# Performance work log

Hardware: AMD Instinct MI355X
Metric: run time of the kernel (lower is better)

Reference implementation:

```python
import jax, jax.numpy as jnp
import numpy as np

N_EMBD = 768
N_HEAD = 12
HEAD_DIM = N_EMBD // N_HEAD  # 64


def setup_inputs() -> dict:
    key = jax.random.key(0)
    k1, k2, k3 = jax.random.split(key, 3)
    B, S = 4, 2048
    x = jax.random.normal(k1, (B, S, N_EMBD), dtype=jnp.float32)
    W_attn = jax.random.normal(k2, (N_EMBD, 3 * N_EMBD), dtype=jnp.float32) * 0.02
    b_attn = jax.random.normal(k3, (3 * N_EMBD,), dtype=jnp.float32) * 0.02
    return {"x": x, "W_attn": W_attn, "b_attn": b_attn}


def reference(x, W_attn, b_attn):
    B, S, E = x.shape
    H, D = N_HEAD, HEAD_DIM
    # fused QKV projection (torch Linear: x @ W^T + b; here W_attn stored as [E, 3E])
    qkv = x @ W_attn + b_attn  # [B, S, 3E]
    q, k, v = jnp.split(qkv, 3, axis=-1)
    q = q.reshape(B, S, H, D)
    k = k.reshape(B, S, H, D)
    v = v.reshape(B, S, H, D)
    scale = 1.0 / np.sqrt(D).astype(np.float32)
    scores = jnp.einsum('bqhd,bkhd->bhqk', q, k) * scale  # [B, H, S, S]
    causal = jnp.tril(jnp.ones((S, S), dtype=bool))
    # ReLU attention nonlinearity (no softmax); masked entries -> 0
    att = jnp.where(causal, jnp.maximum(scores, 0.0), 0.0)
    y = jnp.einsum('bhqk,bkhd->bqhd', att, v)  # [B, S, H, D]
    return y.reshape(B, S, E)
```

## Files before the change

kernel.cpp:

```cpp
#include <hip/hip_runtime.h>

typedef __attribute__((ext_vector_type(8))) short short8;
typedef __attribute__((ext_vector_type(4))) short short4v;
typedef __attribute__((ext_vector_type(4))) float floatx4;
typedef __attribute__((ext_vector_type(2))) unsigned int uint2v;

#define S_LEN 2048
#define NH 12
#define HD 64
#define EMB 768
#define E3 2304

__device__ __forceinline__ unsigned short f2bf(float f) {
    unsigned int u = __builtin_bit_cast(unsigned int, f);
    u += 0x7FFFu + ((u >> 16) & 1u);
    return (unsigned short)(u >> 16);
}

__device__ __forceinline__ unsigned int pack2bf(float a, float b) {
#if __has_builtin(__builtin_amdgcn_cvt_pk_bf16_f32)
    typedef __attribute__((ext_vector_type(2))) short short2v;
    short2v r = __builtin_amdgcn_cvt_pk_bf16_f32(a, b);
    return __builtin_bit_cast(unsigned int, r);
#else
    return (unsigned int)f2bf(a) | ((unsigned int)f2bf(b) << 16);
#endif
}

__device__ __forceinline__ void gl_lds16(const void* g, void* l) {
    __builtin_amdgcn_global_load_lds(
        (const __attribute__((address_space(1))) unsigned int*)g,
        (__attribute__((address_space(3))) unsigned int*)l, 16, 0, 0);
}

__global__ __launch_bounds__(256) void conv_fused(const float* __restrict__ x,
                                                  ushort* __restrict__ xb,
                                                  const float* __restrict__ W,
                                                  ushort* __restrict__ Wt) {
    int tid = threadIdx.x;
    if (blockIdx.x < 6144) {
        int i = (blockIdx.x * 256 + tid) * 4;
        float4 f = *(const float4*)(x + i);
        ushort4 o;
        o.x = f2bf(f.x); o.y = f2bf(f.y); o.z = f2bf(f.z); o.w = f2bf(f.w);
        *(ushort4*)(xb + i) = o;
    } else {
        __shared__ float tile[32][33];
        int b2 = blockIdx.x - 6144;
        int n0 = (b2 % 72) * 32, k0 = (b2 / 72) * 32;
        int tx = tid & 31, ty = tid >> 5;
        for (int i = 0; i < 4; i++)
            tile[ty + i * 8][tx] = W[(size_t)(k0 + ty + i * 8) * E3 + n0 + tx];
        __syncthreads();
        for (int i = 0; i < 4; i++)
            Wt[(size_t)(n0 + ty + i * 8) * EMB + k0 + tx] = f2bf(tile[tx][ty + i * 8]);
    }
}

__global__ __launch_bounds__(256) void qkv_gemm(const ushort* __restrict__ Xb,
                                                const ushort* __restrict__ Wt,
                                                const float* __restrict__ bias,
                                                ushort* __restrict__ QKb,
                                                ushort* __restrict__ Vt) {
    __shared__ ushort lds[16896];
    char* ldsb = (char*)lds;
    int tid  = threadIdx.x;
    int wv = tid >> 6, lane = tid & 63;
    int l15 = lane & 15, quad = lane >> 4;
    int r8 = lane >> 3, cc = lane & 7;
    int wm = wv >> 1, wn = wv & 1;
    int m0 = blockIdx.x * 128, n0 = blockIdx.y * 128;

    floatx4 acc[4][4] = {};

    const char* ag = (const char*)(Xb + (size_t)m0 * EMB)
                   + (wv * 32 + r8) * 1536 + (cc ^ r8) * 16;
    const char* bgp = (const char*)(Wt + (size_t)n0 * EMB)
                   + (wv * 32 + r8) * 1536 + (cc ^ r8) * 16;
    int ast = (wv * 32) * 128;
    int bst = 16384 + (wv * 32) * 128;
    int afo[2], bfo[2];
    for (int ch = 0; ch < 2; ch++) {
        int sw = ((ch * 4 + quad) ^ (l15 & 7)) * 16;
        afo[ch] = wm * 8192 + l15 * 128 + sw;
        bfo[ch] = 16384 + wn * 8192 + l15 * 128 + sw;
    }

    for (int k0 = 0; k0 < 12; k0++) {
        __syncthreads();
        for (int i = 0; i < 4; i++) {
            gl_lds16(ag + i * 12288, ldsb + ast + i * 1024);
            gl_lds16(bgp + i * 12288, ldsb + bst + i * 1024);
        }
        ag += 128;  bgp += 128;
        __syncthreads();
        for (int ch = 0; ch < 2; ch++) {
            short8 af[4], bf[4];
            for (int mi = 0; mi < 4; mi++)
                af[mi] = *(const short8*)(ldsb + afo[ch] + mi * 2048);
            for (int ni = 0; ni < 4; ni++)
                bf[ni] = *(const short8*)(ldsb + bfo[ch] + ni * 2048);
            for (int mi = 0; mi < 4; mi++)
                for (int ni = 0; ni < 4; ni++)
                    acc[mi][ni] = __builtin_amdgcn_mfma_f32_16x16x32_bf16(
                        af[mi], bf[ni], acc[mi][ni], 0, 0, 0);
        }
    }

    __syncthreads();
    int seg = n0 / EMB;
    if (seg < 2) {
        float scale = (seg == 0) ? 0.125f : 1.0f;
        for (int ni = 0; ni < 4; ni++) {
            int nl = wn * 64 + ni * 16 + l15;
            float bv = bias[n0 + nl];
            for (int mi = 0; mi < 4; mi++)
                for (int r = 0; r < 4; r++) {
                    int ml = wm * 64 + mi * 16 + quad * 4 + r;
                    lds[ml * 132 + nl] = f2bf((acc[mi][ni][r] + bv) * scale);
                }
        }
        __syncthreads();
        int row = tid >> 1, half2 = tid & 1;
        size_t gm = (size_t)(m0 + row);
        for (int i = 0; i < 8; i++) {
            uint4 v = *(const uint4*)&lds[row * 132 + half2 * 64 + i * 8];
            *(uint4*)&QKb[gm * 1536 + n0 + half2 * 64 + i * 8] = v;
        }
    } else {
        for (int ni = 0; ni < 4; ni++) {
            int nl = wn * 64 + ni * 16 + l15;
            float bv = bias[n0 + nl];
            for (int mi = 0; mi < 4; mi++) {
                int ml = wm * 64 + mi * 16 + quad * 4;
                ushort4 p4;
                p4.x = f2bf(acc[mi][ni][0] + bv);
                p4.y = f2bf(acc[mi][ni][1] + bv);
                p4.z = f2bf(acc[mi][ni][2] + bv);
                p4.w = f2bf(acc[mi][ni][3] + bv);
                *(ushort4*)&lds[nl * 132 + ml] = p4;
            }
        }
        __syncthreads();
        int row = tid >> 1, half2 = tid & 1;
        int nn = n0 + row - 1536;
        int hh = nn >> 6, d = nn & 63;
        int bb = m0 >> 11, s0 = m0 & 2047;
        for (int i = 0; i < 8; i++) {
            uint4 v = *(const uint4*)&lds[row * 132 + half2 * 64 + i * 8];
            *(uint4*)&Vt[((size_t)(bb * NH + hh) * HD + d) * S_LEN + s0 + half2 * 64 + i * 8] = v;
        }
    }
}

__global__ __launch_bounds__(256) void attn(const ushort* __restrict__ QKb,
                                            const ushort* __restrict__ Vt,
                                            float* __restrict__ out) {
    __shared__ ushort lds[32768];
    char* ldsb = (char*)lds;
    int tid = threadIdx.x;
    int w = tid >> 6, lane = tid & 63;
    int l15 = lane & 15, quad = lane >> 4;
    int r8 = lane >> 3, cc = lane & 7;
    int qh = quad >> 1, qlo = quad & 1;
    int rr = lane >> 4;

    int kfo[2];
    for (int ch = 0; ch < 2; ch++)
        kfo[ch] = l15 * 128 + ((ch * 4 + quad) ^ (l15 & 7)) * 16;
    int vfo[8];
    for (int t = 0; t < 8; t++)
        vfo[t] = 32768 + l15 * 256 + qlo * 8 + ((2 * t + qh) ^ l15) * 16;
    int rhs[2] = { w * 32 + l15, w * 32 + 16 + l15 };
    int kgo = (w * 32 + r8) * 3072 + (cc ^ r8) * 16;
    int vgo[4];
    for (int i = 0; i < 4; i++)
        vgo[i] = (w * 16 + i * 4 + rr) * 4096 + (((lane & 15) ^ ((i * 4 + rr) & 15)) * 16);
    int kst = (w * 32) * 128;
    int vst = 32768 + (w * 16) * 256;

    int b = blockIdx.x;
    int nit, qts[2], bhs[2];
    if (b < 240)      { nit = 1; qts[0] = 15 - b / 48; bhs[0] = b % 48; qts[1] = 0; bhs[1] = 0; }
    else if (b < 480) { int j = b - 240; nit = 2; qts[0] = 10 - j / 48; bhs[0] = j % 48;
                        qts[1] = 1 + j / 48; bhs[1] = j % 48; }
    else              { int j = b - 480; nit = 2; qts[0] = 0; bhs[0] = 2 * j;
                        qts[1] = 0; bhs[1] = 2 * j + 1; }

    const char* kg[2]; const char* vg[2];
    for (int i = 0; i < 2; i++) {
        int bh = bhs[i], bg = bh / NH, h = bh % NH;
        kg[i] = (const char*)(QKb + (size_t)bg * S_LEN * 1536 + 768 + h * 64) + kgo;
        vg[i] = (const char*)(Vt + (size_t)bh * HD * S_LEN);
    }

    auto prefetch = [&](const char* kbase, const char* vbase, int dstP) {
        for (int i = 0; i < 4; i++)
            gl_lds16(kbase + i * 24576, ldsb + dstP * 16384 + kst + i * 1024);
        for (int i = 0; i < 4; i++)
            gl_lds16(vbase + vgo[i], ldsb + dstP * 16384 + vst + i * 1024);
    };

    int p = 0;
    prefetch(kg[0], vg[0], 0);
    for (int ii = 0; ii < nit; ii++) {
        int qt = qts[ii];
        int bh = bhs[ii], bg = bh / NH, h = bh % NH;
        const ushort* Qcol = QKb + (size_t)bg * S_LEN * 1536 + h * 64;
        short8 qf[2][2];
        for (int nq = 0; nq < 2; nq++)
            for (int ch = 0; ch < 2; ch++)
                qf[nq][ch] = *(const short8*)(Qcol +
                    (size_t)(qt * 128 + w * 32 + nq * 16 + l15) * 1536 + ch * 32 + quad * 8);

        floatx4 acco[2][4] = {};
        int nst = qt + 1;
        for (int st = 0; st < nst; st++) {
            __syncthreads();
            if (st + 1 < nst)
                prefetch(kg[ii] + (size_t)(st + 1) * 393216, vg[ii] + (st + 1) * 256, p ^ 1);
            else if (ii + 1 < nit)
                prefetch(kg[ii + 1], vg[ii + 1], p ^ 1);

            bool diag = (st == qt);
            const char* kb = ldsb + p * 16384;

            for (int jsub = 0; jsub < 2; jsub++) {
                floatx4 stc[4][2] = {};
                for (int ch = 0; ch < 2; ch++) {
                    short8 kf[4];
                    for (int mk = 0; mk < 4; mk++)
                        kf[mk] = *(const short8*)(kb + kfo[ch] + jsub * 8192 + mk * 2048);
                    for (int mk = 0; mk < 4; mk++)
                        for (int nq = 0; nq < 2; nq++)
                            stc[mk][nq] = __builtin_amdgcn_mfma_f32_16x16x32_bf16(
                                kf[mk], qf[nq][ch], stc[mk][nq], 0, 0, 0);
                }

                unsigned int pk[4][2][2];
                for (int mk = 0; mk < 4; mk++) {
                    for (int nq = 0; nq < 2; nq++) {
                        float e[4];
                        for (int r = 0; r < 4; r++)
                            e[r] = fmaxf(stc[mk][nq][r], 0.0f);
                        if (diag) {
                            int kl = jsub * 64 + mk * 16 + quad * 4;
                            for (int r = 0; r < 4; r++)
                                if (kl + r > rhs[nq]) e[r] = 0.0f;
                        }
                        pk[mk][nq][0] = pack2bf(e[0], e[1]);
                        pk[mk][nq][1] = pack2bf(e[2], e[3]);
                    }
                }

                for (int mk = 0; mk < 4; mk++) {
                    int t = jsub * 4 + mk;
                    short4v vf[4];
                    for (int ni = 0; ni < 4; ni++)
                        vf[ni] = *(const short4v*)(kb + vfo[t] + ni * 4096);
                    for (int mi = 0; mi < 2; mi++) {
                        short4v a = __builtin_bit_cast(short4v,
                                     (uint2v){pk[mk][mi][0], pk[mk][mi][1]});
                        for (int ni = 0; ni < 4; ni++)
                            acco[mi][ni] = __builtin_amdgcn_mfma_f32_16x16x16bf16_1k(
                                a, vf[ni], acco[mi][ni], 0, 0, 0);
                    }
                }
            }
            p ^= 1;
        }

        for (int mi = 0; mi < 2; mi++) {
            for (int ni = 0; ni < 4; ni++) {
                int d = ni * 16 + l15;
                for (int r = 0; r < 4; r++) {
                    int s = qt * 128 + w * 32 + mi * 16 + quad * 4 + r;
                    out[((size_t)bg * S_LEN + s) * EMB + h * 64 + d] = acco[mi][ni][r];
                }
            }
        }
    }
}

extern "C" void kernel_launch(void* const* d_in, const int* in_sizes, int n_in,
                              void* d_out, int out_size, void* d_ws, size_t ws_size,
                              hipStream_t stream) {
    const float* x    = (const float*)d_in[0];
    const float* W    = (const float*)d_in[1];
    const float* bias = (const float*)d_in[2];
    float* out = (float*)d_out;

    char* ws = (char*)d_ws;
    const size_t SZ_X  = (size_t)8192 * EMB * 2;
    const size_t SZ_W  = (size_t)E3 * EMB * 2;
    const size_t SZ_QK = (size_t)8192 * 1536 * 2;
    ushort* Xb  = (ushort*)(ws);
    ushort* Wt  = (ushort*)(ws + SZ_X);
    ushort* QKb = (ushort*)(ws + SZ_X + SZ_W);
    ushort* Vt  = (ushort*)(ws + SZ_X + SZ_W + SZ_QK);

    conv_fused<<<dim3(6144 + 1728), dim3(256), 0, stream>>>(x, Xb, W, Wt);
    qkv_gemm<<<dim3(64, 18), dim3(256), 0, stream>>>(Xb, Wt, bias, QKb, Vt);
    attn<<<dim3(504), dim3(256), 0, stream>>>(QKb, Vt, out);
}
```

Baseline: 181.5 us.

## Restructure attention into independent per-wave 64-row tiles without block barriers

The attention kernel now launches 768 blocks of two waves each. Each wave owns its own 64-query tile and its own private double-buffered K/V region in LDS. Waves pair a long and a short causal tile (31-g and 15-g) to balance work, and they synchronise with s_waitcnt vmcnt instead of __syncthreads. This removes block-wide barriers and the earlier multi-item scheduling, at the cost of more K/V global loads, since each wave fetches its own copy, and more registers per wave for the larger accumulator tile.

```diff
diff --git a/kernel.cpp b/kernel.cpp
--- a/kernel.cpp
+++ b/kernel.cpp
@@ -153,7 +153,7 @@
     }
 }
 
-__global__ __launch_bounds__(256) void attn(const ushort* __restrict__ QKb,
+__global__ __launch_bounds__(128) void attn(const ushort* __restrict__ QKb,
                                             const ushort* __restrict__ Vt,
                                             float* __restrict__ out) {
     __shared__ ushort lds[32768];
@@ -163,120 +163,98 @@
     int l15 = lane & 15, quad = lane >> 4;
     int r8 = lane >> 3, cc = lane & 7;
     int qh = quad >> 1, qlo = quad & 1;
-    int rr = lane >> 4;
-
+
+    int g = blockIdx.x / 48, bh = blockIdx.x % 48;
+    int qt = w ? (15 - g) : (31 - g);
+    int bg = bh / NH, h = bh % NH;
+
+    const char* Kb = (const char*)(QKb + (size_t)bg * S_LEN * 1536 + 768 + h * 64)
+                   + r8 * 3072 + (cc ^ r8) * 16;
+    const char* Vb = (const char*)(Vt + (size_t)bh * HD * S_LEN)
+                   + r8 * 4096 + (cc ^ r8) * 16;
+    const ushort* Qcol = QKb + (size_t)bg * S_LEN * 1536 + h * 64;
+
+    int wb = w * 32768;
     int kfo[2];
     for (int ch = 0; ch < 2; ch++)
-        kfo[ch] = l15 * 128 + ((ch * 4 + quad) ^ (l15 & 7)) * 16;
-    int vfo[8];
-    for (int t = 0; t < 8; t++)
-        vfo[t] = 32768 + l15 * 256 + qlo * 8 + ((2 * t + qh) ^ l15) * 16;
-    int rhs[2] = { w * 32 + l15, w * 32 + 16 + l15 };
-    int kgo = (w * 32 + r8) * 3072 + (cc ^ r8) * 16;
-    int vgo[4];
-    for (int i = 0; i < 4; i++)
-        vgo[i] = (w * 16 + i * 4 + rr) * 4096 + (((lane & 15) ^ ((i * 4 + rr) & 15)) * 16);
-    int kst = (w * 32) * 128;
-    int vst = 32768 + (w * 16) * 256;
-
-    int b = blockIdx.x;
-    int nit, qts[2], bhs[2];
-    if (b < 240)      { nit = 1; qts[0] = 15 - b / 48; bhs[0] = b % 48; qts[1] = 0; bhs[1] = 0; }
-    else if (b < 480) { int j = b - 240; nit = 2; qts[0] = 10 - j / 48; bhs[0] = j % 48;
-                        qts[1] = 1 + j / 48; bhs[1] = j % 48; }
-    else              { int j = b - 480; nit = 2; qts[0] = 0; bhs[0] = 2 * j;
-                        qts[1] = 0; bhs[1] = 2 * j + 1; }
-
-    const char* kg[2]; const char* vg[2];
-    for (int i = 0; i < 2; i++) {
-        int bh = bhs[i], bg = bh / NH, h = bh % NH;
-        kg[i] = (const char*)(QKb + (size_t)bg * S_LEN * 1536 + 768 + h * 64) + kgo;
-        vg[i] = (const char*)(Vt + (size_t)bh * HD * S_LEN);
-    }
-
-    auto prefetch = [&](const char* kbase, const char* vbase, int dstP) {
-        for (int i = 0; i < 4; i++)
-            gl_lds16(kbase + i * 24576, ldsb + dstP * 16384 + kst + i * 1024);
-        for (int i = 0; i < 4; i++)
-            gl_lds16(vbase + vgo[i], ldsb + dstP * 16384 + vst + i * 1024);
-    };
-
+        kfo[ch] = wb + l15 * 128 + (((ch * 4 + quad) ^ (l15 & 7)) * 16);
+    int vfo[4];
+    for (int kb = 0; kb < 4; kb++)
+        vfo[kb] = wb + 8192 + l15 * 128 + (((kb * 2 + qh) ^ (l15 & 7)) * 16) + qlo * 8;
+
+    for (int i = 0; i < 8; i++)
+        gl_lds16(Kb + i * 24576, ldsb + wb + i * 1024);
+    for (int i = 0; i < 8; i++)
+        gl_lds16(Vb + i * 32768, ldsb + wb + 8192 + i * 1024);
+
+    short8 qf[4][2];
+    for (int nq = 0; nq < 4; nq++)
+        for (int ch = 0; ch < 2; ch++)
+            qf[nq][ch] = *(const short8*)(Qcol +
+                (size_t)(qt * 64 + nq * 16 + l15) * 1536 + ch * 32 + quad * 8);
+
+    floatx4 acco[4][4] = {};
     int p = 0;
-    prefetch(kg[0], vg[0], 0);
-    for (int ii = 0; ii < nit; ii++) {
-        int qt = qts[ii];
-        int bh = bhs[ii], bg = bh / NH, h = bh % NH;
-        const ushort* Qcol = QKb + (size_t)bg * S_LEN * 1536 + h * 64;
-        short8 qf[2][2];
-        for (int nq = 0; nq < 2; nq++)
+    for (int st = 0; st <= qt; st++) {
+        if (st < qt) {
+            const char* ks = Kb + (size_t)(st + 1) * 196608;
+            const char* vs = Vb + (st + 1) * 128;
+            int d = wb + (p ^ 1) * 16384;
+            for (int i = 0; i < 8; i++)
+                gl_lds16(ks + i * 24576, ldsb + d + i * 1024);
+            for (int i = 0; i < 8; i++)
+                gl_lds16(vs + i * 32768, ldsb + d + 8192 + i * 1024);
+            asm volatile("s_waitcnt vmcnt(16)" ::: "memory");
+        } else {
+            asm volatile("s_waitcnt vmcnt(0)" ::: "memory");
+        }
+        int pb = p * 16384;
+        bool diag = (st == qt);
+
+        short4v vf[4][4];
+        for (int kb = 0; kb < 4; kb++)
+            for (int ni = 0; ni < 4; ni++)
+                vf[kb][ni] = *(const short4v*)(ldsb + pb + vfo[kb] + ni * 2048);
+        short8 kf[4][2];
+        for (int mk = 0; mk < 4; mk++)
             for (int ch = 0; ch < 2; ch++)
-                qf[nq][ch] = *(const short8*)(Qcol +
-                    (size_t)(qt * 128 + w * 32 + nq * 16 + l15) * 1536 + ch * 32 + quad * 8);
-
-        floatx4 acco[2][4] = {};
-        int nst = qt + 1;
-        for (int st = 0; st < nst; st++) {
-            __syncthreads();
-            if (st + 1 < nst)
-                prefetch(kg[ii] + (size_t)(st + 1) * 393216, vg[ii] + (st + 1) * 256, p ^ 1);
-            else if (ii + 1 < nit)
-                prefetch(kg[ii + 1], vg[ii + 1], p ^ 1);
-
-            bool diag = (st == qt);
-            const char* kb = ldsb + p * 16384;
-
-            for (int jsub = 0; jsub < 2; jsub++) {
-                floatx4 stc[4][2] = {};
-                for (int ch = 0; ch < 2; ch++) {
-                    short8 kf[4];
-                    for (int mk = 0; mk < 4; mk++)
-                        kf[mk] = *(const short8*)(kb + kfo[ch] + jsub * 8192 + mk * 2048);
-                    for (int mk = 0; mk < 4; mk++)
-                        for (int nq = 0; nq < 2; nq++)
-                            stc[mk][nq] = __builtin_amdgcn_mfma_f32_16x16x32_bf16(
-                                kf[mk], qf[nq][ch], stc[mk][nq], 0, 0, 0);
+                kf[mk][ch] = *(const short8*)(ldsb + pb + kfo[ch] + mk * 2048);
+
+        for (int nq = 0; nq < 4; nq++) {
+            floatx4 stc[4] = {};
+            for (int ch = 0; ch < 2; ch++)
+                for (int mk = 0; mk < 4; mk++)
+                    stc[mk] = __builtin_amdgcn_mfma_f32_16x16x32_bf16(
+                        kf[mk][ch], qf[nq][ch], stc[mk], 0, 0, 0);
+            unsigned int pk[4][2];
+            for (int mk = 0; mk < 4; mk++) {
+                float e[4];
+                for (int r = 0; r < 4; r++) e[r] = fmaxf(stc[mk][r], 0.0f);
+                if (diag) {
+                    int kl = mk * 16 + quad * 4;
+                    int ql = nq * 16 + l15;
+                    for (int r = 0; r < 4; r++)
+                        if (kl + r > ql) e[r] = 0.0f;
                 }
-
-                unsigned int pk[4][2][2];
-                for (int mk = 0; mk < 4; mk++) {
-                    for (int nq = 0; nq < 2; nq++) {
-                        float e[4];
-                        for (int r = 0; r < 4; r++)
-                            e[r] = fmaxf(stc[mk][nq][r], 0.0f);
-                        if (diag) {
-                            int kl = jsub * 64 + mk * 16 + quad * 4;
-                            for (int r = 0; r < 4; r++)
-                                if (kl + r > rhs[nq]) e[r] = 0.0f;
-                        }
-                        pk[mk][nq][0] = pack2bf(e[0], e[1]);
-                        pk[mk][nq][1] = pack2bf(e[2], e[3]);
-                    }
-                }
-
-                for (int mk = 0; mk < 4; mk++) {
-                    int t = jsub * 4 + mk;
-                    short4v vf[4];
-                    for (int ni = 0; ni < 4; ni++)
-                        vf[ni] = *(const short4v*)(kb + vfo[t] + ni * 4096);
-                    for (int mi = 0; mi < 2; mi++) {
-                        short4v a = __builtin_bit_cast(short4v,
-                                     (uint2v){pk[mk][mi][0], pk[mk][mi][1]});
-                        for (int ni = 0; ni < 4; ni++)
-                            acco[mi][ni] = __builtin_amdgcn_mfma_f32_16x16x16bf16_1k(
-                                a, vf[ni], acco[mi][ni], 0, 0, 0);
-                    }
-                }
-            }
-            p ^= 1;
-        }
-
-        for (int mi = 0; mi < 2; mi++) {
-            for (int ni = 0; ni < 4; ni++) {
-                int d = ni * 16 + l15;
-                for (int r = 0; r < 4; r++) {
-                    int s = qt * 128 + w * 32 + mi * 16 + quad * 4 + r;
-                    out[((size_t)bg * S_LEN + s) * EMB + h * 64 + d] = acco[mi][ni][r];
-                }
+                pk[mk][0] = pack2bf(e[0], e[1]);
+                pk[mk][1] = pack2bf(e[2], e[3]);
+            }
+            for (int mk = 0; mk < 4; mk++) {
+                short4v a = __builtin_bit_cast(short4v, (uint2v){pk[mk][0], pk[mk][1]});
+                for (int ni = 0; ni < 4; ni++)
+                    acco[nq][ni] = __builtin_amdgcn_mfma_f32_16x16x16bf16_1k(
+                        a, vf[mk][ni], acco[nq][ni], 0, 0, 0);
+            }
+        }
+        p ^= 1;
+    }
+
+    for (int nq = 0; nq < 4; nq++) {
+        for (int ni = 0; ni < 4; ni++) {
+            int d = ni * 16 + l15;
+            for (int r = 0; r < 4; r++) {
+                int s = qt * 64 + nq * 16 + quad * 4 + r;
+                out[((size_t)bg * S_LEN + s) * EMB + h * 64 + d] = acco[nq][ni][r];
             }
         }
     }
@@ -301,5 +279,5 @@
 
     conv_fused<<<dim3(6144 + 1728), dim3(256), 0, stream>>>(x, Xb, W, Wt);
     qkv_gemm<<<dim3(64, 18), dim3(256), 0, stream>>>(Xb, Wt, bias, QKb, Vt);
-    attn<<<dim3(504), dim3(256), 0, stream>>>(QKb, Vt, out);
-}
+    attn<<<dim3(768), dim3(128), 0, stream>>>(QKb, Vt, out);
+}
```

Result: slower. 202.1 us (+11.4%).
